# Optimization experiments

Hardware: AMD Instinct MI355X
Metric: run time of the kernel (lower is better)

Reference implementation:

```python
import jax, jax.numpy as jnp
import numpy as np


def fps_single(xyz, npoint):
    """Furthest point sampling. xyz: [N,3] -> [npoint] int32 indices (first = 0)."""
    d0 = jnp.sum((xyz - xyz[0]) ** 2, axis=-1)  # [N]

    def body(dists, _):
        nxt = jnp.argmax(dists)
        d = jnp.sum((xyz - xyz[nxt]) ** 2, axis=-1)
        return jnp.minimum(dists, d), nxt.astype(jnp.int32)

    _, idxs = jax.lax.scan(body, d0, None, length=npoint - 1)
    return jnp.concatenate([jnp.zeros((1,), jnp.int32), idxs])


def setup_inputs() -> dict:
    key = jax.random.key(0)
    k1, k2 = jax.random.split(key)
    B, N, C = 4, 8192, 128
    points = jax.random.normal(k1, (B, N, 3), dtype=jnp.float32)
    features = jax.random.normal(k2, (B, C, N), dtype=jnp.float32)
    return {"points": points, "features": features, "npoint": 2048, "nsample": 16}


def reference(points, features, npoint, nsample):
    """FPS downsample -> kNN grouping (mean pool) -> three_nn inverse-distance interpolation.
    points: [B,N,3], features: [B,C,N]. Returns interpolated features [B,C,N]."""
    B, N, _ = points.shape
    # --- furthest point sampling (Sample module) ---
    fps_idx = jax.vmap(lambda p: fps_single(p, npoint))(points)          # [B,Q]
    xyz_q = jnp.take_along_axis(points, fps_idx[..., None], axis=1)      # [B,Q,3]
    # --- pairwise squared distances query->all (pdist2squared) ---
    sq = (jnp.sum(xyz_q ** 2, -1)[:, :, None]
          + jnp.sum(points ** 2, -1)[:, None, :]
          - 2.0 * jnp.einsum('bqd,bnd->bqn', xyz_q, points))             # [B,Q,N]
    sq = jnp.maximum(sq, 0.0)
    # --- kNN neighbors, drop self (SampleNeighbors, knn=True takes topk nsample+1 then [:,:,1:]) ---
    _, nbr = jax.lax.top_k(-sq, nsample + 1)                             # [B,Q,K+1]
    nbr = nbr[..., 1:]                                                   # [B,Q,K]
    grouped = jax.vmap(lambda f, idx: f[:, idx])(features, nbr)          # [B,C,Q,K]
    coarse = jnp.mean(grouped, axis=-1)                                  # [B,C,Q]
    # --- three_nn + inverse squared-distance interpolation (GraphFPModule) ---
    neg_d3, i3 = jax.lax.top_k(-jnp.swapaxes(sq, 1, 2), 3)               # [B,N,3]
    d3 = jnp.maximum(-neg_d3, 1e-10)                                     # squared dists, clamped
    inv = 1.0 / (d3 + 1e-8)
    w = inv / jnp.sum(inv, axis=-1, keepdims=True)                       # [B,N,3]
    f3 = jax.vmap(lambda f, idx: f[:, idx])(coarse, i3)                  # [B,C,N,3]
    out = jnp.sum(f3 * w[:, None, :, :], axis=-1)                        # [B,C,N]
    return out
```

## Files before the change

### kernel.cpp

```cpp
#include <hip/hip_runtime.h>
#include <cstdint>
#include <cstddef>

#define Bq   4
#define Nq   8192
#define Cq   128
#define NPq  2048
#define KSEL 17

typedef float v2f __attribute__((ext_vector_type(2)));

__device__ __forceinline__ float rn_sq3(float x, float y, float z) {
  return __fadd_rn(__fadd_rn(__fmul_rn(x, x), __fmul_rn(y, y)), __fmul_rn(z, z));
}

__device__ __forceinline__ v2f dist2_v2(v2f px, v2f py, v2f pz, float cx, float cy, float cz) {
#pragma clang fp contract(off)
  v2f dx = px - cx;
  v2f dy = py - cy;
  v2f dz = pz - cz;
  v2f s = dx * dx + dy * dy + dz * dz;
  return s;
}

__device__ __forceinline__ float sq_expand(float qx, float qy, float qz, float sq_,
                                           float px, float py, float pz, float sp_) {
  float dot = __fadd_rn(__fadd_rn(__fmul_rn(qx, px), __fmul_rn(qy, py)), __fmul_rn(qz, pz));
  float v = __fsub_rn(__fadd_rn(sq_, sp_), __fmul_rn(2.0f, dot));
  v = fmaxf(v, 0.0f);
  return __fadd_rn(v, 0.0f);
}

__global__ __launch_bounds__(256) void k_sump(const float* __restrict__ pts,
                                              float* __restrict__ sump) {
  int g = blockIdx.x * 256 + threadIdx.x;
  float x = pts[g * 3 + 0], y = pts[g * 3 + 1], z = pts[g * 3 + 2];
  sump[g] = rn_sq3(x, y, z);
}

template <int CTRL, int RM, int BM>
__device__ __forceinline__ float dpp_maxf(float v) {
  int r = __builtin_amdgcn_update_dpp(__float_as_int(v), __float_as_int(v), CTRL, RM, BM, false);
  return fmaxf(v, __int_as_float(r));
}

__global__ __launch_bounds__(512) void k_fps(const float* __restrict__ pts,
                                             int* __restrict__ fps_idx) {
  const int b = blockIdx.x;
  const int tid = threadIdx.x;
  const int lane = tid & 63, wid = tid >> 6;
  const float* P = pts + (size_t)b * Nq * 3;

  __shared__ float sv[2][8];
  __shared__ int spi[2][8];

  v2f px[8], py[8], pz[8], dd[8];
  const int pbase = tid * 16;
#pragma unroll
  for (int j = 0; j < 8; j++) {
    const float2* q2 = (const float2*)(P + (size_t)(pbase + 2 * j) * 3);
    float2 A = q2[0], Bv = q2[1], Cv = q2[2];
    v2f tx, ty, tz;
    tx.x = A.x;  tx.y = Bv.y;
    ty.x = A.y;  ty.y = Cv.x;
    tz.x = Bv.x; tz.y = Cv.y;
    px[j] = tx; py[j] = ty; pz[j] = tz;
  }
  float qx = P[0], qy = P[1], qz = P[2];
  float bd = -1.0f;
  int bp = pbase;
#pragma unroll
  for (int j = 0; j < 8; j++) {
    v2f s = dist2_v2(px[j], py[j], pz[j], qx, qy, qz);
    dd[j] = s;
    if (s.x > bd) { bd = s.x; bp = pbase + 2 * j; }
    if (s.y > bd) { bd = s.y; bp = pbase + 2 * j + 1; }
  }
  if (tid == 0) fps_idx[b * NPq] = 0;

  for (int i = 1; i < NPq; i++) {
    float wv = bd;
    wv = dpp_maxf<0x111, 0xf, 0xf>(wv);
    wv = dpp_maxf<0x112, 0xf, 0xf>(wv);
    wv = dpp_maxf<0x114, 0xf, 0xf>(wv);
    wv = dpp_maxf<0x118, 0xf, 0xf>(wv);
    wv = dpp_maxf<0x142, 0xa, 0xf>(wv);
    wv = dpp_maxf<0x143, 0xc, 0xf>(wv);
    float wmax = __int_as_float(__builtin_amdgcn_readlane(__float_as_int(wv), 63));
    unsigned long long msk = __ballot(bd == wmax);
    int wl = (int)__ffsll(msk) - 1;
    int wbp = __shfl(bp, wl);
    if (lane == 0) { sv[i & 1][wid] = wmax; spi[i & 1][wid] = wbp; }
    __syncthreads();

    float bv = sv[i & 1][0];
    int bip = spi[i & 1][0];
#pragma unroll
    for (int w = 1; w < 8; w++) {
      float tv = sv[i & 1][w];
      bool t = tv > bv;
      bv = t ? tv : bv;
      bip = t ? spi[i & 1][w] : bip;
    }
    if (tid == 0) fps_idx[b * NPq + i] = bip;

    const float* cp = P + (size_t)bip * 3;
    float cx = cp[0], cy = cp[1], cz = cp[2];

    bd = -1.0f;
    bp = pbase;
#pragma unroll
    for (int j = 0; j < 8; j++) {
      v2f s = dist2_v2(px[j], py[j], pz[j], cx, cy, cz);
      v2f nd;
      nd.x = fminf(dd[j].x, s.x);
      nd.y = fminf(dd[j].y, s.y);
      dd[j] = nd;
      if (nd.x > bd) { bd = nd.x; bp = pbase + 2 * j; }
      if (nd.y > bd) { bd = nd.y; bp = pbase + 2 * j + 1; }
    }
  }
}

__global__ __launch_bounds__(256) void k_gatherq(const float* __restrict__ pts,
                                                 const float* __restrict__ sump,
                                                 const int* __restrict__ fps_idx,
                                                 float* __restrict__ xyzq,
                                                 float* __restrict__ sumq,
                                                 float* __restrict__ xqs,
                                                 float* __restrict__ yqs,
                                                 float* __restrict__ zqs) {
  int g = blockIdx.x * 256 + threadIdx.x;
  int b = g >> 11;
  int idx = fps_idx[g];
  int src = b * Nq + idx;
  float x = pts[src * 3 + 0], y = pts[src * 3 + 1], z = pts[src * 3 + 2];
  xyzq[g * 3 + 0] = x;
  xyzq[g * 3 + 1] = y;
  xyzq[g * 3 + 2] = z;
  xqs[g] = x; yqs[g] = y; zqs[g] = z;
  sumq[g] = sump[src];
}

__global__ __launch_bounds__(256) void k_knn_group(const float* __restrict__ pts,
                                                   const float* __restrict__ sump,
                                                   const float* __restrict__ xyzq,
                                                   const float* __restrict__ sumq,
                                                   const float* __restrict__ feats,
                                                   float* __restrict__ coarse_t) {
  const int blk = blockIdx.x;
  const int b = blk >> 11;
  const int tid = threadIdx.x;
  const int lane = tid & 63, wid = tid >> 6;
  const float* P = pts + (size_t)b * Nq * 3;
  const float* SP = sump + (size_t)b * Nq;

  __shared__ float sq_lds[Nq];
  __shared__ unsigned long long wk[2][4];
  __shared__ int sel[KSEL];

  float qx = xyzq[blk * 3 + 0], qy = xyzq[blk * 3 + 1], qz = xyzq[blk * 3 + 2];
  float sq_ = sumq[blk];

  unsigned long long lmin = ~0ull;
#pragma unroll
  for (int k = 0; k < 32; k++) {
    int p = k * 256 + tid;
    float x = P[p * 3 + 0], y = P[p * 3 + 1], z = P[p * 3 + 2];
    float v = sq_expand(qx, qy, qz, sq_, x, y, z, SP[p]);
    sq_lds[p] = v;
    unsigned long long key = ((unsigned long long)__float_as_uint(v) << 32) | (unsigned int)p;
    lmin = key < lmin ? key : lmin;
  }

  for (int r = 0; r < KSEL; r++) {
    unsigned long long key = lmin;
#pragma unroll
    for (int off = 32; off > 0; off >>= 1) {
      unsigned long long o = __shfl_down(key, off);
      key = o < key ? o : key;
    }
    if (lane == 0) wk[r & 1][wid] = key;
    __syncthreads();
    unsigned long long m = wk[r & 1][0];
    m = wk[r & 1][1] < m ? wk[r & 1][1] : m;
    m = wk[r & 1][2] < m ? wk[r & 1][2] : m;
    m = wk[r & 1][3] < m ? wk[r & 1][3] : m;
    int p = (int)(unsigned int)(m & 0xFFFFFFFFull);
    if (tid == 0) sel[r] = p;
    if ((p & 255) == tid) {
      sq_lds[p] = __uint_as_float(0x7f800000u);
      lmin = ~0ull;
#pragma unroll
      for (int k = 0; k < 32; k++) {
        int pp = k * 256 + tid;
        unsigned long long kk =
            ((unsigned long long)__float_as_uint(sq_lds[pp]) << 32) | (unsigned int)pp;
        lmin = kk < lmin ? kk : lmin;
      }
    }
  }
  __syncthreads();

  if (tid < Cq) {
    const float* F = feats + ((size_t)(b * Cq + tid)) * Nq;
    float acc = 0.0f;
#pragma unroll
    for (int j = 1; j < KSEL; j++) acc += F[sel[j]];
    coarse_t[(size_t)blk * Cq + tid] = acc * (1.0f / 16.0f);
  }
}

__device__ __forceinline__ void merge3(unsigned long long& a0, unsigned long long& a1,
                                       unsigned long long& a2, unsigned long long b0,
                                       unsigned long long b1, unsigned long long b2) {
  unsigned long long lo1 = a0 < b0 ? a0 : b0;
  unsigned long long hi1 = a0 < b0 ? b0 : a0;
  unsigned long long lo2 = a1 < b1 ? a1 : b1;
  unsigned long long hi2 = a1 < b1 ? b1 : a1;
  unsigned long long lo3 = a2 < b2 ? a2 : b2;
  unsigned long long c1 = hi1 < lo2 ? hi1 : lo2;
  unsigned long long m1 = hi1 < lo2 ? lo2 : hi1;
  unsigned long long m2 = hi2 < lo3 ? hi2 : lo3;
  a0 = lo1;
  a1 = c1;
  a2 = m1 < m2 ? m1 : m2;
}

__global__ __launch_bounds__(256) void k_three(const float* __restrict__ pts,
                                               const float* __restrict__ sump,
                                               const float* __restrict__ xqs,
                                               const float* __restrict__ yqs,
                                               const float* __restrict__ zqs,
                                               const float* __restrict__ sumq,
                                               int* __restrict__ i0, int* __restrict__ i1,
                                               int* __restrict__ i2, float* __restrict__ w0,
                                               float* __restrict__ w1, float* __restrict__ w2) {
  const int wid = threadIdx.x >> 6, lane = threadIdx.x & 63;
  const int n = blockIdx.x * 4 + wid;
  const int b = n >> 13;
  float px = pts[n * 3 + 0], py = pts[n * 3 + 1], pz = pts[n * 3 + 2];
  float sp = sump[n];
  const float* QX = xqs + (size_t)b * NPq;
  const float* QY = yqs + (size_t)b * NPq;
  const float* QZ = zqs + (size_t)b * NPq;
  const float* SQ = sumq + (size_t)b * NPq;

  unsigned long long k0 = ~0ull, k1 = ~0ull, k2 = ~0ull;
#pragma unroll 4
  for (int j = 0; j < 32; j++) {
    int q = lane + j * 64;
    float v = sq_expand(QX[q], QY[q], QZ[q], SQ[q], px, py, pz, sp);
    unsigned long long key = ((unsigned long long)__float_as_uint(v) << 32) | (unsigned int)q;
    if (key < k2) {
      if (key < k1) {
        k2 = k1;
        if (key < k0) { k1 = k0; k0 = key; } else { k1 = key; }
      } else {
        k2 = key;
      }
    }
  }
#pragma unroll
  for (int off = 32; off > 0; off >>= 1) {
    unsigned long long o0 = __shfl_down(k0, off);
    unsigned long long o1 = __shfl_down(k1, off);
    unsigned long long o2 = __shfl_down(k2, off);
    merge3(k0, k1, k2, o0, o1, o2);
  }
  if (lane == 0) {
    float v0 = __uint_as_float((unsigned int)(k0 >> 32));
    float v1 = __uint_as_float((unsigned int)(k1 >> 32));
    float v2 = __uint_as_float((unsigned int)(k2 >> 32));
    float d0 = fmaxf(v0, 1e-10f), d1 = fmaxf(v1, 1e-10f), d2 = fmaxf(v2, 1e-10f);
    float inv0 = 1.0f / (d0 + 1e-8f);
    float inv1 = 1.0f / (d1 + 1e-8f);
    float inv2 = 1.0f / (d2 + 1e-8f);
    float s = inv0 + inv1 + inv2;
    i0[n] = (int)(unsigned int)(k0 & 0xFFFFFFFFull);
    i1[n] = (int)(unsigned int)(k1 & 0xFFFFFFFFull);
    i2[n] = (int)(unsigned int)(k2 & 0xFFFFFFFFull);
    w0[n] = inv0 / s;
    w1[n] = inv1 / s;
    w2[n] = inv2 / s;
  }
}

__global__ __launch_bounds__(256) void k_interp(const float* __restrict__ coarse_t,
                                                const int* __restrict__ i0,
                                                const int* __restrict__ i1,
                                                const int* __restrict__ i2,
                                                const float* __restrict__ w0,
                                                const float* __restrict__ w1,
                                                const float* __restrict__ w2,
                                                float* __restrict__ out) {
  int g = blockIdx.x * 256 + threadIdx.x;
  int b = g >> 13, n = g & (Nq - 1);
  int a0 = i0[g], a1 = i1[g], a2 = i2[g];
  float u0 = w0[g], u1 = w1[g], u2 = w2[g];
  const float4* r0 = (const float4*)(coarse_t + ((size_t)b * NPq + a0) * Cq);
  const float4* r1 = (const float4*)(coarse_t + ((size_t)b * NPq + a1) * Cq);
  const float4* r2 = (const float4*)(coarse_t + ((size_t)b * NPq + a2) * Cq);
  float* O = out + (size_t)b * Cq * Nq + n;
#pragma unroll 4
  for (int cq = 0; cq < Cq / 4; cq++) {
    float4 f0 = r0[cq], f1 = r1[cq], f2 = r2[cq];
    float o0 = u0 * f0.x + u1 * f1.x + u2 * f2.x;
    float o1 = u0 * f0.y + u1 * f1.y + u2 * f2.y;
    float o2 = u0 * f0.z + u1 * f1.z + u2 * f2.z;
    float o3 = u0 * f0.w + u1 * f1.w + u2 * f2.w;
    O[(size_t)(cq * 4 + 0) * Nq] = o0;
    O[(size_t)(cq * 4 + 1) * Nq] = o1;
    O[(size_t)(cq * 4 + 2) * Nq] = o2;
    O[(size_t)(cq * 4 + 3) * Nq] = o3;
  }
}

extern "C" void kernel_launch(void* const* d_in, const int* in_sizes, int n_in,
                              void* d_out, int out_size, void* d_ws, size_t ws_size,
                              hipStream_t stream) {
  const float* pts = (const float*)d_in[0];
  const float* feats = (const float*)d_in[1];
  float* out = (float*)d_out;

  char* ws = (char*)d_ws;
  size_t off = 0;
  auto alloc = [&](size_t bytes) {
    void* p = ws + off;
    off += (bytes + 255) & ~(size_t)255;
    return p;
  };
  float* sump = (float*)alloc((size_t)Bq * Nq * 4);
  int* fps_idx = (int*)alloc((size_t)Bq * NPq * 4);
  float* xyzq = (float*)alloc((size_t)Bq * NPq * 3 * 4);
  float* sumq = (float*)alloc((size_t)Bq * NPq * 4);
  float* coarse_t = (float*)alloc((size_t)Bq * NPq * Cq * 4);
  int* i0 = (int*)alloc((size_t)Bq * Nq * 4);
  int* i1 = (int*)alloc((size_t)Bq * Nq * 4);
  int* i2 = (int*)alloc((size_t)Bq * Nq * 4);
  float* w0 = (float*)alloc((size_t)Bq * Nq * 4);
  float* w1 = (float*)alloc((size_t)Bq * Nq * 4);
  float* w2 = (float*)alloc((size_t)Bq * Nq * 4);
  float* xqs = (float*)alloc((size_t)Bq * NPq * 4);
  float* yqs = (float*)alloc((size_t)Bq * NPq * 4);
  float* zqs = (float*)alloc((size_t)Bq * NPq * 4);

  k_sump<<<(Bq * Nq) / 256, 256, 0, stream>>>(pts, sump);
  k_fps<<<Bq, 512, 0, stream>>>(pts, fps_idx);
  k_gatherq<<<(Bq * NPq) / 256, 256, 0, stream>>>(pts, sump, fps_idx, xyzq, sumq, xqs, yqs, zqs);
  k_knn_group<<<Bq * NPq, 256, 0, stream>>>(pts, sump, xyzq, sumq, feats, coarse_t);
  k_three<<<(Bq * Nq) / 4, 256, 0, stream>>>(pts, sump, xqs, yqs, zqs, sumq, i0, i1, i2, w0, w1, w2);
  k_interp<<<(Bq * Nq) / 256, 256, 0, stream>>>(coarse_t, i0, i1, i2, w0, w1, w2, out);
}
```

Before: 2.412 ms.

## Shorten FPS iteration critical path and pack point xyz+norm for kNN loads

The FPS loop now tracks only the running max value per thread and recovers the argmax index lazily in the winning lane. It reduces the eight wave results with xor-shuffles instead of a serial loop and reads the chosen centroid from LDS copies of the coordinates instead of global memory. A new packed float4 buffer (x,y,z,|p|^2) written by k_sump lets the kNN kernel do one vector load per point instead of four scalar loads. The aim is to cut per-iteration latency in the serial 2048-step FPS loop and memory transactions in kNN, at the cost of 96KB extra LDS in k_fps, an extra workspace buffer, and a tie-break path that must preserve first-index semantics.

After: 2.520 ms. 1.04x slower.

```diff
diff --git a/kernel.cpp b/kernel.cpp
--- a/kernel.cpp
+++ b/kernel.cpp
@@ -32,10 +32,13 @@
 }
 
 __global__ __launch_bounds__(256) void k_sump(const float* __restrict__ pts,
-                                              float* __restrict__ sump) {
+                                              float* __restrict__ sump,
+                                              float4* __restrict__ pxyzs) {
   int g = blockIdx.x * 256 + threadIdx.x;
   float x = pts[g * 3 + 0], y = pts[g * 3 + 1], z = pts[g * 3 + 2];
-  sump[g] = rn_sq3(x, y, z);
+  float s = rn_sq3(x, y, z);
+  sump[g] = s;
+  pxyzs[g] = make_float4(x, y, z, s);
 }
 
 template <int CTRL, int RM, int BM>
@@ -51,6 +54,7 @@
   const int lane = tid & 63, wid = tid >> 6;
   const float* P = pts + (size_t)b * Nq * 3;
 
+  __shared__ float ldsx[Nq], ldsy[Nq], ldsz[Nq];
   __shared__ float sv[2][8];
   __shared__ int spi[2][8];
 
@@ -65,17 +69,21 @@
     ty.x = A.y;  ty.y = Cv.x;
     tz.x = Bv.x; tz.y = Cv.y;
     px[j] = tx; py[j] = ty; pz[j] = tz;
+    ldsx[pbase + 2 * j] = tx.x; ldsx[pbase + 2 * j + 1] = tx.y;
+    ldsy[pbase + 2 * j] = ty.x; ldsy[pbase + 2 * j + 1] = ty.y;
+    ldsz[pbase + 2 * j] = tz.x; ldsz[pbase + 2 * j + 1] = tz.y;
   }
   float qx = P[0], qy = P[1], qz = P[2];
-  float bd = -1.0f;
-  int bp = pbase;
+  v2f bdv;
+  bdv.x = -1.0f; bdv.y = -1.0f;
 #pragma unroll
   for (int j = 0; j < 8; j++) {
     v2f s = dist2_v2(px[j], py[j], pz[j], qx, qy, qz);
     dd[j] = s;
-    if (s.x > bd) { bd = s.x; bp = pbase + 2 * j; }
-    if (s.y > bd) { bd = s.y; bp = pbase + 2 * j + 1; }
-  }
+    bdv.x = fmaxf(bdv.x, s.x);
+    bdv.y = fmaxf(bdv.y, s.y);
+  }
+  float bd = fmaxf(bdv.x, bdv.y);
   if (tid == 0) fps_idx[b * NPq] = 0;
 
   for (int i = 1; i < NPq; i++) {
@@ -89,26 +97,34 @@
     float wmax = __int_as_float(__builtin_amdgcn_readlane(__float_as_int(wv), 63));
     unsigned long long msk = __ballot(bd == wmax);
     int wl = (int)__ffsll(msk) - 1;
-    int wbp = __shfl(bp, wl);
-    if (lane == 0) { sv[i & 1][wid] = wmax; spi[i & 1][wid] = wbp; }
+    if (lane == wl) {
+      int kk = 15;
+#pragma unroll
+      for (int j = 7; j >= 0; j--) {
+        if (dd[j].y == wmax) kk = 2 * j + 1;
+        if (dd[j].x == wmax) kk = 2 * j;
+      }
+      sv[i & 1][wid] = wmax;
+      spi[i & 1][wid] = pbase + kk;
+    }
     __syncthreads();
 
-    float bv = sv[i & 1][0];
-    int bip = spi[i & 1][0];
-#pragma unroll
-    for (int w = 1; w < 8; w++) {
-      float tv = sv[i & 1][w];
-      bool t = tv > bv;
-      bv = t ? tv : bv;
-      bip = t ? spi[i & 1][w] : bip;
-    }
+    float v = sv[i & 1][lane & 7];
+    int slot = lane & 7;
+#pragma unroll
+    for (int off = 1; off < 8; off <<= 1) {
+      float ov = __shfl_xor(v, off);
+      int os = __shfl_xor(slot, off);
+      bool take = (ov > v) || (ov == v && os < slot);
+      v = take ? ov : v;
+      slot = take ? os : slot;
+    }
+    int bip = spi[i & 1][slot];
     if (tid == 0) fps_idx[b * NPq + i] = bip;
 
-    const float* cp = P + (size_t)bip * 3;
-    float cx = cp[0], cy = cp[1], cz = cp[2];
-
-    bd = -1.0f;
-    bp = pbase;
+    float cx = ldsx[bip], cy = ldsy[bip], cz = ldsz[bip];
+
+    bdv.x = -1.0f; bdv.y = -1.0f;
 #pragma unroll
     for (int j = 0; j < 8; j++) {
       v2f s = dist2_v2(px[j], py[j], pz[j], cx, cy, cz);
@@ -116,9 +132,10 @@
       nd.x = fminf(dd[j].x, s.x);
       nd.y = fminf(dd[j].y, s.y);
       dd[j] = nd;
-      if (nd.x > bd) { bd = nd.x; bp = pbase + 2 * j; }
-      if (nd.y > bd) { bd = nd.y; bp = pbase + 2 * j + 1; }
-    }
+      bdv.x = fmaxf(bdv.x, nd.x);
+      bdv.y = fmaxf(bdv.y, nd.y);
+    }
+    bd = fmaxf(bdv.x, bdv.y);
   }
 }
 
@@ -142,8 +159,7 @@
   sumq[g] = sump[src];
 }
 
-__global__ __launch_bounds__(256) void k_knn_group(const float* __restrict__ pts,
-                                                   const float* __restrict__ sump,
+__global__ __launch_bounds__(256) void k_knn_group(const float4* __restrict__ pxyzs,
                                                    const float* __restrict__ xyzq,
                                                    const float* __restrict__ sumq,
                                                    const float* __restrict__ feats,
@@ -152,8 +168,7 @@
   const int b = blk >> 11;
   const int tid = threadIdx.x;
   const int lane = tid & 63, wid = tid >> 6;
-  const float* P = pts + (size_t)b * Nq * 3;
-  const float* SP = sump + (size_t)b * Nq;
+  const float4* PS = pxyzs + (size_t)b * Nq;
 
   __shared__ float sq_lds[Nq];
   __shared__ unsigned long long wk[2][4];
@@ -166,8 +181,8 @@
 #pragma unroll
   for (int k = 0; k < 32; k++) {
     int p = k * 256 + tid;
-    float x = P[p * 3 + 0], y = P[p * 3 + 1], z = P[p * 3 + 2];
-    float v = sq_expand(qx, qy, qz, sq_, x, y, z, SP[p]);
+    float4 t = PS[p];
+    float v = sq_expand(qx, qy, qz, sq_, t.x, t.y, t.z, t.w);
     sq_lds[p] = v;
     unsigned long long key = ((unsigned long long)__float_as_uint(v) << 32) | (unsigned int)p;
     lmin = key < lmin ? key : lmin;
@@ -331,6 +346,7 @@
     return p;
   };
   float* sump = (float*)alloc((size_t)Bq * Nq * 4);
+  float4* pxyzs = (float4*)alloc((size_t)Bq * Nq * 16);
   int* fps_idx = (int*)alloc((size_t)Bq * NPq * 4);
   float* xyzq = (float*)alloc((size_t)Bq * NPq * 3 * 4);
   float* sumq = (float*)alloc((size_t)Bq * NPq * 4);
@@ -345,10 +361,10 @@
   float* yqs = (float*)alloc((size_t)Bq * NPq * 4);
   float* zqs = (float*)alloc((size_t)Bq * NPq * 4);
 
-  k_sump<<<(Bq * Nq) / 256, 256, 0, stream>>>(pts, sump);
+  k_sump<<<(Bq * Nq) / 256, 256, 0, stream>>>(pts, sump, pxyzs);
   k_fps<<<Bq, 512, 0, stream>>>(pts, fps_idx);
   k_gatherq<<<(Bq * NPq) / 256, 256, 0, stream>>>(pts, sump, fps_idx, xyzq, sumq, xqs, yqs, zqs);
-  k_knn_group<<<Bq * NPq, 256, 0, stream>>>(pts, sump, xyzq, sumq, feats, coarse_t);
+  k_knn_group<<<Bq * NPq, 256, 0, stream>>>(pxyzs, xyzq, sumq, feats, coarse_t);
   k_three<<<(Bq * Nq) / 4, 256, 0, stream>>>(pts, sump, xqs, yqs, zqs, sumq, i0, i1, i2, w0, w1, w2);
   k_interp<<<(Bq * Nq) / 256, 256, 0, stream>>>(coarse_t, i0, i1, i2, w0, w1, w2, out);
 }
```
